# Kernel optimization log

Measured on AMD Instinct MI355X. Metric: run time of the kernel, lower is better.

## Reference

```python
import jax, jax.numpy as jnp
import numpy as np

N_ITERS = 3  # Set2Set n_iters


def _set2set(feat, gid, B, Wih, Whh, bih, bhh):
    # DGL Set2Set with n_iters=3, n_layers=1: LSTM(input=2D, hidden=D), PyTorch gate order i,f,g,o
    N, D = feat.shape
    q_star = jnp.zeros((B, 2 * D), feat.dtype)
    h = jnp.zeros((B, D), feat.dtype)
    c = jnp.zeros((B, D), feat.dtype)
    bias = bih + bhh
    for _ in range(N_ITERS):
        gates = q_star @ Wih.T + h @ Whh.T + bias  # (B, 4D)
        i, f, g, o = jnp.split(gates, 4, axis=-1)
        i = jax.nn.sigmoid(i); f = jax.nn.sigmoid(f); o = jax.nn.sigmoid(o); g = jnp.tanh(g)
        c = f * c + i * g
        h = o * jnp.tanh(c)  # q = h, shape (B, D)
        e = jnp.sum(feat * h[gid], axis=-1)  # (N,) attention logits
        m = jax.ops.segment_max(e, gid, num_segments=B, indices_are_sorted=True)
        ex = jnp.exp(e - m[gid])
        s = jax.ops.segment_sum(ex, gid, num_segments=B, indices_are_sorted=True)
        alpha = ex / s[gid]  # segment softmax
        readout = jax.ops.segment_sum(feat * alpha[:, None], gid, num_segments=B, indices_are_sorted=True)
        q_star = jnp.concatenate([h, readout], axis=-1)  # (B, 2D)
    return q_star


def setup_inputs() -> dict:
    key = jax.random.key(0)
    ks = jax.random.split(key, 18)
    N, E, D, B, OUT = 100000, 1000000, 64, 64, 1
    s = 1.0 / np.sqrt(D)
    u = lambda k, shp, b: jax.random.uniform(k, shp, jnp.float32, -b, b)
    inp = {
        'feat': jax.random.normal(ks[0], (N, D), jnp.float32),
        'efeat': jax.random.normal(ks[1], (E, D), jnp.float32),
        'edge_dst': jax.random.randint(ks[2], (E,), 0, N, jnp.int32),
        'node_graph': jnp.sort(jax.random.randint(ks[3], (N,), 0, B, jnp.int32)),
        'n_graphs': B,
        'node_Wih': u(ks[4], (4 * D, 2 * D), s), 'node_Whh': u(ks[5], (4 * D, D), s),
        'node_bih': u(ks[6], (4 * D,), s), 'node_bhh': u(ks[7], (4 * D,), s),
        'edge_Wih': u(ks[8], (4 * D, 2 * D), s), 'edge_Whh': u(ks[9], (4 * D, D), s),
        'edge_bih': u(ks[10], (4 * D,), s), 'edge_bhh': u(ks[11], (4 * D,), s),
        'W1': u(ks[12], (32, 4 * D), np.sqrt(6.0 / (4 * D + 32)) * np.sqrt(2.0)),
        'b1': jnp.zeros((32,), jnp.float32),
        'W2': u(ks[13], (16, 32), np.sqrt(6.0 / 48) * np.sqrt(2.0)),
        'b2': jnp.zeros((16,), jnp.float32),
        'W3': u(ks[14], (OUT, 16), np.sqrt(6.0 / (16 + OUT)) * np.sqrt(2.0)),
        'b3': jnp.zeros((OUT,), jnp.float32),
    }
    return inp


def reference(feat, efeat, edge_dst, node_graph, n_graphs,
              node_Wih, node_Whh, node_bih, node_bhh,
              edge_Wih, edge_Whh, edge_bih, edge_bhh,
              W1, b1, W2, b2, W3, b3):
    N = feat.shape[0]
    # mpnn = identity: node_emb = feat, edge_emb = efeat
    node_s2s = _set2set(feat, node_graph, n_graphs, node_Wih, node_Whh, node_bih, node_bhh)
    # graph.update_all(fn.copy_e, fn.mean): scatter-mean of edge features onto dst nodes
    deg = jax.ops.segment_sum(jnp.ones((efeat.shape[0],), feat.dtype), edge_dst, num_segments=N)
    edge_agg = jax.ops.segment_sum(efeat, edge_dst, num_segments=N) / jnp.maximum(deg, 1.0)[:, None]
    edge_s2s = _set2set(edge_agg, node_graph, n_graphs, edge_Wih, edge_Whh, edge_bih, edge_bhh)
    out = jnp.concatenate([node_s2s, edge_s2s], axis=1)  # (B, 4D)
    out = jax.nn.relu(out @ W1.T + b1)
    out = jax.nn.relu(out @ W2.T + b2)
    out = out @ W3.T + b3
    return out
```

## Files before the change

kernel.cpp:

```cpp
#include <hip/hip_runtime.h>
#include <math.h>

#define D 64
#define B 64
#define NPB 256
#define SCAN_BS 1024

__device__ __forceinline__ unsigned encf(float x) {
  unsigned u = __float_as_uint(x);
  return (u & 0x80000000u) ? ~u : (u | 0x80000000u);
}
__device__ __forceinline__ float decf(unsigned e) {
  return (e & 0x80000000u) ? __uint_as_float(e ^ 0x80000000u) : __uint_as_float(~e);
}
__device__ __forceinline__ float sigm(float x) { return 1.0f / (1.0f + expf(-x)); }


__global__ void k_deg(const int* __restrict__ edge_dst, int* __restrict__ deg, int E) {
  int i = blockIdx.x * blockDim.x + threadIdx.x;
  if (i < E) atomicAdd(&deg[edge_dst[i]], 1);
}

__global__ void k_scan1(const int* __restrict__ deg, int* __restrict__ row_start,
                        int* __restrict__ blocksum, int N) {
  __shared__ int sm[SCAN_BS];
  int t = threadIdx.x;
  int base = blockIdx.x * SCAN_BS;
  int v = (base + t < N) ? deg[base + t] : 0;
  sm[t] = v;
  __syncthreads();
  for (int ofs = 1; ofs < SCAN_BS; ofs <<= 1) {
    int add = (t >= ofs) ? sm[t - ofs] : 0;
    __syncthreads();
    sm[t] += add;
    __syncthreads();
  }
  if (base + t < N) row_start[base + t] = sm[t] - v;
  if (t == SCAN_BS - 1) blocksum[blockIdx.x] = sm[t];
}

__global__ void k_scan2(int* __restrict__ blocksum, int nb) {
  __shared__ int sm[128];
  int t = threadIdx.x;
  int v = (t < nb) ? blocksum[t] : 0;
  sm[t] = v;
  __syncthreads();
  for (int ofs = 1; ofs < 128; ofs <<= 1) {
    int add = (t >= ofs) ? sm[t - ofs] : 0;
    __syncthreads();
    sm[t] += add;
    __syncthreads();
  }
  if (t < nb) blocksum[t] = sm[t] - v;
}

__global__ void k_scan3(int* __restrict__ row_start, const int* __restrict__ blocksum,
                        int* __restrict__ cursor, int N) {
  int n = blockIdx.x * blockDim.x + threadIdx.x;
  if (n < N) {
    int v = row_start[n] + blocksum[n / SCAN_BS];
    row_start[n] = v;
    cursor[n] = v;
  }
}

__global__ void k_fill(const int* __restrict__ edge_dst, int* __restrict__ cursor,
                       int* __restrict__ csr, int E) {
  int e = blockIdx.x * blockDim.x + threadIdx.x;
  if (e < E) {
    int dst = edge_dst[e];
    int idx = atomicAdd(&cursor[dst], 1);
    csr[idx] = e;
  }
}

__global__ void k_gather(const float* __restrict__ efeat, const int* __restrict__ csr,
                         const int* __restrict__ row_start, const int* __restrict__ deg,
                         float* __restrict__ edge_agg, int N) {
  int grp = (blockIdx.x * blockDim.x + threadIdx.x) >> 4;
  int l16 = threadIdx.x & 15;
  if (grp >= N) return;
  int base = row_start[grp];
  int dg = deg[grp];
  float4 acc = make_float4(0.f, 0.f, 0.f, 0.f);
  for (int i = 0; i < dg; i += 16) {
    int idx[16];
    #pragma unroll
    for (int j = 0; j < 16; ++j) {
      int k = i + j;
      idx[j] = csr[base + (k < dg ? k : dg - 1)];
    }
    #pragma unroll
    for (int j = 0; j < 16; ++j) {
      float4 v = *(const float4*)(efeat + (size_t)idx[j] * D + l16 * 4);
      bool ok = (i + j < dg);
      acc.x += ok ? v.x : 0.0f;
      acc.y += ok ? v.y : 0.0f;
      acc.z += ok ? v.z : 0.0f;
      acc.w += ok ? v.w : 0.0f;
    }
  }
  float inv = 1.0f / fmaxf((float)dg, 1.0f);
  acc.x *= inv; acc.y *= inv; acc.z *= inv; acc.w *= inv;
  *(float4*)(edge_agg + (size_t)grp * D + l16 * 4) = acc;
}


__global__ void k_lstm2(int first, float* __restrict__ h2, float* __restrict__ c2,
                        float* __restrict__ s2, float* __restrict__ r2,
                        unsigned* __restrict__ m2, float* __restrict__ off2,
                        const float* __restrict__ nWih, const float* __restrict__ nWhh,
                        const float* __restrict__ nbih, const float* __restrict__ nbhh,
                        const float* __restrict__ eWih, const float* __restrict__ eWhh,
                        const float* __restrict__ ebih, const float* __restrict__ ebhh) {
  __shared__ float sq[2 * D], sh[D], sg[4 * D];
  int side = blockIdx.y;
  const float* Wih = side ? eWih : nWih;
  const float* Whh = side ? eWhh : nWhh;
  const float* bih = side ? ebih : nbih;
  const float* bhh = side ? ebhh : nbhh;
  float* h = h2 + side * B * D;
  float* c = c2 + side * B * D;
  float* s_buf = s2 + side * B;
  float* r_buf = r2 + side * B * D;

  int b = blockIdx.x, j = threadIdx.x;
  if (j < D) {
    float hv = h[b * D + j];
    sq[j] = hv;
    sh[j] = hv;
  } else if (j < 2 * D) {
    sq[j] = first ? 0.0f : (r_buf[b * D + (j - D)] / s_buf[b]);
  }
  __syncthreads();
  float acc = bih[j] + bhh[j];
  const float* wr = Wih + (size_t)j * (2 * D);
  #pragma unroll 8
  for (int k = 0; k < 2 * D; ++k) acc += sq[k] * wr[k];
  const float* wr2 = Whh + (size_t)j * D;
  #pragma unroll 8
  for (int k = 0; k < D; ++k) acc += sh[k] * wr2[k];
  sg[j] = acc;
  __syncthreads();
  if (j < D) {
    float ig = sigm(sg[j]);
    float fg = sigm(sg[D + j]);
    float gg = tanhf(sg[2 * D + j]);
    float og = sigm(sg[3 * D + j]);
    float cn = fg * c[b * D + j] + ig * gg;
    c[b * D + j] = cn;
    h[b * D + j] = og * tanhf(cn);
    r_buf[b * D + j] = 0.0f;
  }
  if (j == D) s_buf[b] = 0.0f;
  if (j == D + 1) {
    int idx = side * B + b;
    off2[idx] = first ? 0.0f : decf(m2[idx]);
    m2[idx] = 0u;
  }
}

#define NSLOT 4
__global__ void k_att_fused(const float* __restrict__ feat, const float* __restrict__ edge_agg,
                            const int* __restrict__ gid, const float* __restrict__ h2,
                            const float* __restrict__ off2, unsigned* __restrict__ m2,
                            float* __restrict__ s2, float* __restrict__ r2, int N) {
  __shared__ float r_lds[16 * NSLOT * D];
  __shared__ float s_lds[16 * NSLOT];
  __shared__ float m_lds[16 * NSLOT];
  __shared__ float h_lds[NSLOT * D];
  __shared__ float o_lds[NSLOT];
  __shared__ int sg_first;
  __shared__ int used[NSLOT];

  int side = blockIdx.y;
  const float* F = side ? edge_agg : feat;
  const float* h = h2 + side * B * D;
  const float* off = off2 + side * B;
  unsigned* m_enc = m2 + side * B;
  float* s_buf = s2 + side * B;
  float* r_buf = r2 + side * B * D;

  int tid = threadIdx.x;
  int grp = tid >> 4;
  int d4  = tid & 15;
  int base = blockIdx.x * NPB;

  for (int i = tid; i < 16 * NSLOT * D; i += 256) r_lds[i] = 0.0f;
  if (tid < 16 * NSLOT) { s_lds[tid] = 0.0f; m_lds[tid] = -3.4e38f; }
  if (tid < NSLOT) used[tid] = 0;
  if (tid == 0) sg_first = gid[base];
  __syncthreads();
  int gfirst = sg_first;
  {
    int slot = tid >> 6, dim = tid & 63;
    int g = gfirst + slot;
    if (g < B) {
      h_lds[tid] = h[g * D + dim];
      if (dim == 0) o_lds[slot] = off[g];
    }
  }
  __syncthreads();

  float4 acc = make_float4(0.f, 0.f, 0.f, 0.f);
  float sum_ex = 0.0f;
  float local_max = -3.4e38f;
  int cur_g = -1;


  for (int it = 0; it < NPB / 32; ++it) {
    int n0 = base + it * 32 + grp;
    int n1 = n0 + 16;
    bool ok0 = n0 < N, ok1 = n1 < N;
    int g0 = ok0 ? gid[n0] : -1;
    int g1 = ok1 ? gid[n1] : -1;
    float4 f0 = make_float4(0,0,0,0), f1 = make_float4(0,0,0,0);
    float dot0 = 0.f, dot1 = 0.f, ex0 = 0.f, ex1 = 0.f;
    if (ok0) {
      f0 = *(const float4*)(F + (size_t)n0 * D + d4 * 4);
      int s0 = g0 - gfirst;
      float4 hv = (s0 >= 0 && s0 < NSLOT) ? *(const float4*)&h_lds[(s0 << 6) + (d4 << 2)]
                                          : *(const float4*)(h + (size_t)g0 * D + d4 * 4);
      dot0 = f0.x * hv.x + f0.y * hv.y + f0.z * hv.z + f0.w * hv.w;
    }
    if (ok1) {
      f1 = *(const float4*)(F + (size_t)n1 * D + d4 * 4);
      int s1 = g1 - gfirst;
      float4 hv = (s1 >= 0 && s1 < NSLOT) ? *(const float4*)&h_lds[(s1 << 6) + (d4 << 2)]
                                          : *(const float4*)(h + (size_t)g1 * D + d4 * 4);
      dot1 = f1.x * hv.x + f1.y * hv.y + f1.z * hv.z + f1.w * hv.w;
    }
    dot0 += __shfl_xor(dot0, 1); dot1 += __shfl_xor(dot1, 1);
    dot0 += __shfl_xor(dot0, 2); dot1 += __shfl_xor(dot1, 2);
    dot0 += __shfl_xor(dot0, 4); dot1 += __shfl_xor(dot1, 4);
    dot0 += __shfl_xor(dot0, 8); dot1 += __shfl_xor(dot1, 8);
    if (ok0) {
      int s0 = g0 - gfirst;
      ex0 = expf(dot0 - ((s0 >= 0 && s0 < NSLOT) ? o_lds[s0] : off[g0]));
    }
    if (ok1) {
      int s1 = g1 - gfirst;
      ex1 = expf(dot1 - ((s1 >= 0 && s1 < NSLOT) ? o_lds[s1] : off[g1]));
    }

    #pragma unroll
    for (int pair = 0; pair < 2; ++pair) {
      bool ok = pair ? ok1 : ok0;
      int g = pair ? g1 : g0;
      float ex = pair ? ex1 : ex0;
      float dt = pair ? dot1 : dot0;
      float4 f = pair ? f1 : f0;
      if (!ok) continue;
      if (g != cur_g) {
        if (cur_g >= 0) {
          int slot = cur_g - gfirst;
          if (slot >= 0 && slot < NSLOT) {
            float4* p = (float4*)&r_lds[((grp * NSLOT + slot) << 6) + (d4 << 2)];
            float4 v = *p;
            v.x += acc.x; v.y += acc.y; v.z += acc.z; v.w += acc.w;
            *p = v;
            if (d4 == 0) {
              s_lds[grp * NSLOT + slot] += sum_ex;
              m_lds[grp * NSLOT + slot] = fmaxf(m_lds[grp * NSLOT + slot], local_max);
              used[slot] = 1;
            }
          } else {
            float* rp = r_buf + cur_g * D + d4 * 4;
            atomicAdd(rp + 0, acc.x); atomicAdd(rp + 1, acc.y);
            atomicAdd(rp + 2, acc.z); atomicAdd(rp + 3, acc.w);
            if (d4 == 0) { atomicAdd(&s_buf[cur_g], sum_ex); atomicMax(&m_enc[cur_g], encf(local_max)); }
          }
        }
        cur_g = g; acc = make_float4(0,0,0,0); sum_ex = 0.f; local_max = -3.4e38f;
      }
      acc.x += ex * f.x; acc.y += ex * f.y; acc.z += ex * f.z; acc.w += ex * f.w;
      if (d4 == 0) { sum_ex += ex; local_max = fmaxf(local_max, dt); }
    }
  }
  if (cur_g >= 0) {
    int slot = cur_g - gfirst;
    if (slot >= 0 && slot < NSLOT) {
      float4* p = (float4*)&r_lds[((grp * NSLOT + slot) << 6) + (d4 << 2)];
      float4 v = *p;
      v.x += acc.x; v.y += acc.y; v.z += acc.z; v.w += acc.w;
      *p = v;
      if (d4 == 0) {
        s_lds[grp * NSLOT + slot] += sum_ex;
        m_lds[grp * NSLOT + slot] = fmaxf(m_lds[grp * NSLOT + slot], local_max);
        used[slot] = 1;
      }
    } else {
      float* rp = r_buf + cur_g * D + d4 * 4;
      atomicAdd(rp + 0, acc.x); atomicAdd(rp + 1, acc.y);
      atomicAdd(rp + 2, acc.z); atomicAdd(rp + 3, acc.w);
      if (d4 == 0) { atomicAdd(&s_buf[cur_g], sum_ex); atomicMax(&m_enc[cur_g], encf(local_max)); }
    }
  }
  __syncthreads();

  {
    int slot = tid >> 6, dim = tid & 63;
    int g = gfirst + slot;
    if (g < B && used[slot]) {
      float sum = 0.0f;
      #pragma unroll
      for (int q = 0; q < 16; ++q) sum += r_lds[((q * NSLOT + slot) << 6) + dim];
      atomicAdd(&r_buf[g * D + dim], sum);
    }
  }
  if (tid < NSLOT) {
    int g = gfirst + tid;
    if (g < B && used[tid]) {
      float ssum = 0.0f;
      #pragma unroll
      for (int q = 0; q < 16; ++q) ssum += s_lds[q * NSLOT + tid];
      atomicAdd(&s_buf[g], ssum);
    }
  } else if (tid >= 64 && tid < 64 + NSLOT) {
    int slot = tid - 64;
    int g = gfirst + slot;
    if (g < B && used[slot]) {
      float mmax = -3.4e38f;
      #pragma unroll
      for (int q = 0; q < 16; ++q) mmax = fmaxf(mmax, m_lds[q * NSLOT + slot]);
      atomicMax(&m_enc[g], encf(mmax));
    }
  }
}

__global__ void k_mlp(const float* __restrict__ h2, const float* __restrict__ r2,
                      const float* __restrict__ s2,
                      const float* __restrict__ W1, const float* __restrict__ b1,
                      const float* __restrict__ W2, const float* __restrict__ b2,
                      const float* __restrict__ W3, const float* __restrict__ b3,
                      float* __restrict__ out) {
  __shared__ float x[4 * D], h1[32], h2s[16];
  int b = blockIdx.x, t = threadIdx.x;
  x[t]       = (t < D) ? h2[b * D + t]         : r2[b * D + (t - D)] / s2[b];
  x[128 + t] = (t < D) ? h2[B * D + b * D + t] : r2[B * D + b * D + (t - D)] / s2[B + b];
  __syncthreads();
  if (t < 32) {
    float acc = b1[t];
    const float* w = W1 + (size_t)t * (4 * D);
    #pragma unroll 8
    for (int k = 0; k < 4 * D; ++k) acc += x[k] * w[k];
    h1[t] = fmaxf(acc, 0.0f);
  }
  __syncthreads();
  if (t < 16) {
    float acc = b2[t];
    const float* w = W2 + (size_t)t * 32;
    #pragma unroll
    for (int k = 0; k < 32; ++k) acc += h1[k] * w[k];
    h2s[t] = fmaxf(acc, 0.0f);
  }
  __syncthreads();
  if (t == 0) {
    float acc = b3[0];
    #pragma unroll
    for (int k = 0; k < 16; ++k) acc += h2s[k] * W3[k];
    out[b] = acc;
  }
}


extern "C" void kernel_launch(void* const* d_in, const int* in_sizes, int n_in,
                              void* d_out, int out_size, void* d_ws, size_t ws_size,
                              hipStream_t stream) {
  const float* feat      = (const float*)d_in[0];
  const float* efeat     = (const float*)d_in[1];
  const int*   edge_dst  = (const int*)d_in[2];
  const int*   node_graph= (const int*)d_in[3];
  const float* node_Wih  = (const float*)d_in[5];
  const float* node_Whh  = (const float*)d_in[6];
  const float* node_bih  = (const float*)d_in[7];
  const float* node_bhh  = (const float*)d_in[8];
  const float* edge_Wih  = (const float*)d_in[9];
  const float* edge_Whh  = (const float*)d_in[10];
  const float* edge_bih  = (const float*)d_in[11];
  const float* edge_bhh  = (const float*)d_in[12];
  const float* W1 = (const float*)d_in[13];
  const float* b1 = (const float*)d_in[14];
  const float* W2 = (const float*)d_in[15];
  const float* b2 = (const float*)d_in[16];
  const float* W3 = (const float*)d_in[17];
  const float* b3 = (const float*)d_in[18];
  float* out = (float*)d_out;

  const int N = in_sizes[0] / D;
  const int E = in_sizes[2];

  float* ws = (float*)d_ws;
  size_t off = 0;
  float* edge_agg = ws + off; off += (size_t)N * D;
  float* h2       = ws + off; off += 2 * B * D;
  float* c2       = ws + off; off += 2 * B * D;
  float* s2       = ws + off; off += 2 * B;
  float* r2       = ws + off; off += 2 * B * D;
  float* off2     = ws + off; off += 2 * B;
  unsigned* m2    = (unsigned*)(ws + off); off += 2 * B;
  int* deg        = (int*)(ws + off); off += N;
  int* row_start  = (int*)(ws + off); off += N;
  int* cursor     = (int*)(ws + off); off += N;
  int* blocksum   = (int*)(ws + off); off += 128;
  int* csr        = (int*)(ws + off); off += E + 8;

  hipMemsetAsync(deg, 0, (size_t)N * sizeof(int), stream);
  hipMemsetAsync(h2, 0, (size_t)(4 * B * D) * sizeof(float), stream);

  const int nb = (N + SCAN_BS - 1) / SCAN_BS;
  k_deg<<<(E + 255) / 256, 256, 0, stream>>>(edge_dst, deg, E);
  k_scan1<<<nb, SCAN_BS, 0, stream>>>(deg, row_start, blocksum, N);
  k_scan2<<<1, 128, 0, stream>>>(blocksum, nb);
  k_scan3<<<(N + 255) / 256, 256, 0, stream>>>(row_start, blocksum, cursor, N);
  k_fill<<<(E + 255) / 256, 256, 0, stream>>>(edge_dst, cursor, csr, E);

  k_gather<<<(N + 15) / 16, 256, 0, stream>>>(efeat, csr, row_start, deg, edge_agg, N);

  const int att_blocks = (N + NPB - 1) / NPB;
  dim3 ga(att_blocks, 2), gb(B, 2);

  for (int it = 0; it < 3; ++it) {
    k_lstm2<<<gb, 256, 0, stream>>>(it == 0 ? 1 : 0, h2, c2, s2, r2, m2, off2,
                                    node_Wih, node_Whh, node_bih, node_bhh,
                                    edge_Wih, edge_Whh, edge_bih, edge_bhh);
    k_att_fused<<<ga, 256, 0, stream>>>(feat, edge_agg, node_graph, h2, off2, m2, s2, r2, N);
  }

  k_mlp<<<B, 128, 0, stream>>>(h2, r2, s2, W1, b1, W2, b2, W3, b3, out);
}
```

Before: 267.5 us.

## Fuse Set2Set LSTM, attention and MLP into one cooperative kernel

Replaces the three pairs of LSTM and attention launches plus the final MLP launch with a single cooperative kernel that uses grid-wide syncs between phases. NPB doubles to 512 so the grid (196x2 blocks) can stay co-resident under launch_bounds(256,2). This removes six kernel launches and their gaps. In exchange it adds grid barrier cost, requires every block to be resident at once, and gives each block twice as much serial work.

```diff
diff --git a/kernel.cpp b/kernel.cpp
--- a/kernel.cpp
+++ b/kernel.cpp
@@ -1,9 +1,13 @@
 #include <hip/hip_runtime.h>
+#include <hip/hip_cooperative_groups.h>
 #include <math.h>
+
+namespace cg = cooperative_groups;
 
 #define D 64
 #define B 64
-#define NPB 256
+#define NPB 512
+#define NSLOT 4
 #define SCAN_BS 1024
 
 __device__ __forceinline__ unsigned encf(float x) {
@@ -106,260 +110,264 @@
 }
 
 
-__global__ void k_lstm2(int first, float* __restrict__ h2, float* __restrict__ c2,
-                        float* __restrict__ s2, float* __restrict__ r2,
-                        unsigned* __restrict__ m2, float* __restrict__ off2,
-                        const float* __restrict__ nWih, const float* __restrict__ nWhh,
-                        const float* __restrict__ nbih, const float* __restrict__ nbhh,
-                        const float* __restrict__ eWih, const float* __restrict__ eWhh,
-                        const float* __restrict__ ebih, const float* __restrict__ ebhh) {
-  __shared__ float sq[2 * D], sh[D], sg[4 * D];
-  int side = blockIdx.y;
+__global__ __launch_bounds__(256, 2)
+void k_s2s(const float* __restrict__ feat, const float* __restrict__ edge_agg,
+           const int* __restrict__ gid,
+           float* __restrict__ h2g, float* __restrict__ c2g,
+           float* __restrict__ s2g, float* __restrict__ r2g,
+           unsigned* __restrict__ m2g, float* __restrict__ off2g,
+           const float* __restrict__ nWih, const float* __restrict__ nWhh,
+           const float* __restrict__ nbih, const float* __restrict__ nbhh,
+           const float* __restrict__ eWih, const float* __restrict__ eWhh,
+           const float* __restrict__ ebih, const float* __restrict__ ebhh,
+           const float* __restrict__ W1, const float* __restrict__ b1,
+           const float* __restrict__ W2, const float* __restrict__ b2,
+           const float* __restrict__ W3, const float* __restrict__ b3,
+           float* __restrict__ out, int N) {
+  cg::grid_group gg = cg::this_grid();
+
+  const int side = blockIdx.y;
+  const int bx = blockIdx.x;
+  const int tid = threadIdx.x;
+
+  const float* F   = side ? edge_agg : feat;
   const float* Wih = side ? eWih : nWih;
   const float* Whh = side ? eWhh : nWhh;
   const float* bih = side ? ebih : nbih;
   const float* bhh = side ? ebhh : nbhh;
-  float* h = h2 + side * B * D;
-  float* c = c2 + side * B * D;
-  float* s_buf = s2 + side * B;
-  float* r_buf = r2 + side * B * D;
-
-  int b = blockIdx.x, j = threadIdx.x;
-  if (j < D) {
-    float hv = h[b * D + j];
-    sq[j] = hv;
-    sh[j] = hv;
-  } else if (j < 2 * D) {
-    sq[j] = first ? 0.0f : (r_buf[b * D + (j - D)] / s_buf[b]);
-  }
-  __syncthreads();
-  float acc = bih[j] + bhh[j];
-  const float* wr = Wih + (size_t)j * (2 * D);
-  #pragma unroll 8
-  for (int k = 0; k < 2 * D; ++k) acc += sq[k] * wr[k];
-  const float* wr2 = Whh + (size_t)j * D;
-  #pragma unroll 8
-  for (int k = 0; k < D; ++k) acc += sh[k] * wr2[k];
-  sg[j] = acc;
-  __syncthreads();
-  if (j < D) {
-    float ig = sigm(sg[j]);
-    float fg = sigm(sg[D + j]);
-    float gg = tanhf(sg[2 * D + j]);
-    float og = sigm(sg[3 * D + j]);
-    float cn = fg * c[b * D + j] + ig * gg;
-    c[b * D + j] = cn;
-    h[b * D + j] = og * tanhf(cn);
-    r_buf[b * D + j] = 0.0f;
-  }
-  if (j == D) s_buf[b] = 0.0f;
-  if (j == D + 1) {
-    int idx = side * B + b;
-    off2[idx] = first ? 0.0f : decf(m2[idx]);
-    m2[idx] = 0u;
-  }
-}
-
-#define NSLOT 4
-__global__ void k_att_fused(const float* __restrict__ feat, const float* __restrict__ edge_agg,
-                            const int* __restrict__ gid, const float* __restrict__ h2,
-                            const float* __restrict__ off2, unsigned* __restrict__ m2,
-                            float* __restrict__ s2, float* __restrict__ r2, int N) {
+  float* h     = h2g + side * B * D;
+  float* c     = c2g + side * B * D;
+  float* s_buf = s2g + side * B;
+  float* r_buf = r2g + side * B * D;
+  unsigned* m_enc = m2g + side * B;
+  float* off   = off2g + side * B;
+
   __shared__ float r_lds[16 * NSLOT * D];
   __shared__ float s_lds[16 * NSLOT];
   __shared__ float m_lds[16 * NSLOT];
   __shared__ float h_lds[NSLOT * D];
   __shared__ float o_lds[NSLOT];
+  __shared__ int used[NSLOT];
   __shared__ int sg_first;
-  __shared__ int used[NSLOT];
-
-  int side = blockIdx.y;
-  const float* F = side ? edge_agg : feat;
-  const float* h = h2 + side * B * D;
-  const float* off = off2 + side * B;
-  unsigned* m_enc = m2 + side * B;
-  float* s_buf = s2 + side * B;
-  float* r_buf = r2 + side * B * D;
-
-  int tid = threadIdx.x;
-  int grp = tid >> 4;
-  int d4  = tid & 15;
-  int base = blockIdx.x * NPB;
-
-  for (int i = tid; i < 16 * NSLOT * D; i += 256) r_lds[i] = 0.0f;
-  if (tid < 16 * NSLOT) { s_lds[tid] = 0.0f; m_lds[tid] = -3.4e38f; }
-  if (tid < NSLOT) used[tid] = 0;
-  if (tid == 0) sg_first = gid[base];
-  __syncthreads();
-  int gfirst = sg_first;
-  {
-    int slot = tid >> 6, dim = tid & 63;
-    int g = gfirst + slot;
-    if (g < B) {
-      h_lds[tid] = h[g * D + dim];
-      if (dim == 0) o_lds[slot] = off[g];
-    }
-  }
-  __syncthreads();
-
-  float4 acc = make_float4(0.f, 0.f, 0.f, 0.f);
-  float sum_ex = 0.0f;
-  float local_max = -3.4e38f;
-  int cur_g = -1;
-
-
-  for (int it = 0; it < NPB / 32; ++it) {
-    int n0 = base + it * 32 + grp;
-    int n1 = n0 + 16;
-    bool ok0 = n0 < N, ok1 = n1 < N;
-    int g0 = ok0 ? gid[n0] : -1;
-    int g1 = ok1 ? gid[n1] : -1;
-    float4 f0 = make_float4(0,0,0,0), f1 = make_float4(0,0,0,0);
-    float dot0 = 0.f, dot1 = 0.f, ex0 = 0.f, ex1 = 0.f;
-    if (ok0) {
-      f0 = *(const float4*)(F + (size_t)n0 * D + d4 * 4);
-      int s0 = g0 - gfirst;
-      float4 hv = (s0 >= 0 && s0 < NSLOT) ? *(const float4*)&h_lds[(s0 << 6) + (d4 << 2)]
-                                          : *(const float4*)(h + (size_t)g0 * D + d4 * 4);
-      dot0 = f0.x * hv.x + f0.y * hv.y + f0.z * hv.z + f0.w * hv.w;
-    }
-    if (ok1) {
-      f1 = *(const float4*)(F + (size_t)n1 * D + d4 * 4);
-      int s1 = g1 - gfirst;
-      float4 hv = (s1 >= 0 && s1 < NSLOT) ? *(const float4*)&h_lds[(s1 << 6) + (d4 << 2)]
-                                          : *(const float4*)(h + (size_t)g1 * D + d4 * 4);
-      dot1 = f1.x * hv.x + f1.y * hv.y + f1.z * hv.z + f1.w * hv.w;
-    }
-    dot0 += __shfl_xor(dot0, 1); dot1 += __shfl_xor(dot1, 1);
-    dot0 += __shfl_xor(dot0, 2); dot1 += __shfl_xor(dot1, 2);
-    dot0 += __shfl_xor(dot0, 4); dot1 += __shfl_xor(dot1, 4);
-    dot0 += __shfl_xor(dot0, 8); dot1 += __shfl_xor(dot1, 8);
-    if (ok0) {
-      int s0 = g0 - gfirst;
-      ex0 = expf(dot0 - ((s0 >= 0 && s0 < NSLOT) ? o_lds[s0] : off[g0]));
-    }
-    if (ok1) {
-      int s1 = g1 - gfirst;
-      ex1 = expf(dot1 - ((s1 >= 0 && s1 < NSLOT) ? o_lds[s1] : off[g1]));
-    }
-
-    #pragma unroll
-    for (int pair = 0; pair < 2; ++pair) {
-      bool ok = pair ? ok1 : ok0;
-      int g = pair ? g1 : g0;
-      float ex = pair ? ex1 : ex0;
-      float dt = pair ? dot1 : dot0;
-      float4 f = pair ? f1 : f0;
-      if (!ok) continue;
-      if (g != cur_g) {
-        if (cur_g >= 0) {
-          int slot = cur_g - gfirst;
-          if (slot >= 0 && slot < NSLOT) {
-            float4* p = (float4*)&r_lds[((grp * NSLOT + slot) << 6) + (d4 << 2)];
-            float4 v = *p;
-            v.x += acc.x; v.y += acc.y; v.z += acc.z; v.w += acc.w;
-            *p = v;
-            if (d4 == 0) {
-              s_lds[grp * NSLOT + slot] += sum_ex;
-              m_lds[grp * NSLOT + slot] = fmaxf(m_lds[grp * NSLOT + slot], local_max);
-              used[slot] = 1;
+  __shared__ float lq[2 * D];
+  __shared__ float lsg[4 * D];
+
+  const int base = bx * NPB;
+  const int grp = tid >> 4;
+  const int d4  = tid & 15;
+
+  for (int it = 0; it < 3; ++it) {
+    if (bx < B) {
+      const int b = bx, j = tid;
+      if (j < D) {
+        lq[j] = h[b * D + j];
+      } else if (j < 2 * D) {
+        lq[j] = (it == 0) ? 0.0f : (r_buf[b * D + (j - D)] / s_buf[b]);
+      }
+      __syncthreads();
+      float acc = bih[j] + bhh[j];
+      const float* wr = Wih + (size_t)j * (2 * D);
+      #pragma unroll 8
+      for (int k = 0; k < 2 * D; ++k) acc += lq[k] * wr[k];
+      const float* wr2 = Whh + (size_t)j * D;
+      #pragma unroll 8
+      for (int k = 0; k < D; ++k) acc += lq[k] * wr2[k];
+      lsg[j] = acc;
+      __syncthreads();
+      if (j < D) {
+        float ig = sigm(lsg[j]);
+        float fg = sigm(lsg[D + j]);
+        float gGate = tanhf(lsg[2 * D + j]);
+        float og = sigm(lsg[3 * D + j]);
+        float cn = fg * c[b * D + j] + ig * gGate;
+        c[b * D + j] = cn;
+        h[b * D + j] = og * tanhf(cn);
+        r_buf[b * D + j] = 0.0f;
+      }
+      if (j == D) s_buf[b] = 0.0f;
+      if (j == D + 1) {
+        off[b] = (it == 0) ? 0.0f : decf(m_enc[b]);
+        m_enc[b] = 0u;
+      }
+      __syncthreads();
+    }
+    gg.sync();
+
+    for (int i = tid; i < 16 * NSLOT * D; i += 256) r_lds[i] = 0.0f;
+    if (tid < 16 * NSLOT) { s_lds[tid] = 0.0f; m_lds[tid] = -3.4e38f; }
+    if (tid < NSLOT) used[tid] = 0;
+    if (tid == 0) sg_first = gid[base];
+    __syncthreads();
+    const int gfirst = sg_first;
+    {
+      int slot = tid >> 6, dim = tid & 63;
+      int g = gfirst + slot;
+      if (g < B) {
+        h_lds[tid] = h[g * D + dim];
+        if (dim == 0) o_lds[slot] = off[g];
+      }
+    }
+    __syncthreads();
+
+    float4 acc = make_float4(0.f, 0.f, 0.f, 0.f);
+    float sum_ex = 0.0f;
+    float local_max = -3.4e38f;
+    int cur_g = -1;
+
+    for (int itn = 0; itn < NPB / 32; ++itn) {
+      int n0 = base + itn * 32 + grp;
+      int n1 = n0 + 16;
+      bool ok0 = n0 < N, ok1 = n1 < N;
+      int g0 = ok0 ? gid[n0] : -1;
+      int g1 = ok1 ? gid[n1] : -1;
+      float4 f0 = make_float4(0,0,0,0), f1 = make_float4(0,0,0,0);
+      float dot0 = 0.f, dot1 = 0.f, ex0 = 0.f, ex1 = 0.f;
+      if (ok0) {
+        f0 = *(const float4*)(F + (size_t)n0 * D + d4 * 4);
+        int s0 = g0 - gfirst;
+        float4 hv = (s0 >= 0 && s0 < NSLOT) ? *(const float4*)&h_lds[(s0 << 6) + (d4 << 2)]
+                                            : *(const float4*)(h + (size_t)g0 * D + d4 * 4);
+        dot0 = f0.x * hv.x + f0.y * hv.y + f0.z * hv.z + f0.w * hv.w;
+      }
+      if (ok1) {
+        f1 = *(const float4*)(F + (size_t)n1 * D + d4 * 4);
+        int s1 = g1 - gfirst;
+        float4 hv = (s1 >= 0 && s1 < NSLOT) ? *(const float4*)&h_lds[(s1 << 6) + (d4 << 2)]
+                                            : *(const float4*)(h + (size_t)g1 * D + d4 * 4);
+        dot1 = f1.x * hv.x + f1.y * hv.y + f1.z * hv.z + f1.w * hv.w;
+      }
+      dot0 += __shfl_xor(dot0, 1); dot1 += __shfl_xor(dot1, 1);
+      dot0 += __shfl_xor(dot0, 2); dot1 += __shfl_xor(dot1, 2);
+      dot0 += __shfl_xor(dot0, 4); dot1 += __shfl_xor(dot1, 4);
+      dot0 += __shfl_xor(dot0, 8); dot1 += __shfl_xor(dot1, 8);
+      if (ok0) {
+        int s0 = g0 - gfirst;
+        ex0 = expf(dot0 - ((s0 >= 0 && s0 < NSLOT) ? o_lds[s0] : off[g0]));
+      }
+      if (ok1) {
+        int s1 = g1 - gfirst;
+        ex1 = expf(dot1 - ((s1 >= 0 && s1 < NSLOT) ? o_lds[s1] : off[g1]));
+      }
+
+      #pragma unroll
+      for (int pair = 0; pair < 2; ++pair) {
+        bool ok = pair ? ok1 : ok0;
+        int g = pair ? g1 : g0;
+        float ex = pair ? ex1 : ex0;
+        float dt = pair ? dot1 : dot0;
+        float4 f = pair ? f1 : f0;
+        if (!ok) continue;
+        if (g != cur_g) {
+          if (cur_g >= 0) {
+            int slot = cur_g - gfirst;
+            if (slot >= 0 && slot < NSLOT) {
+              float4* p = (float4*)&r_lds[((grp * NSLOT + slot) << 6) + (d4 << 2)];
+              float4 v = *p;
+              v.x += acc.x; v.y += acc.y; v.z += acc.z; v.w += acc.w;
+              *p = v;
+              if (d4 == 0) {
+                s_lds[grp * NSLOT + slot] += sum_ex;
+                m_lds[grp * NSLOT + slot] = fmaxf(m_lds[grp * NSLOT + slot], local_max);
+                used[slot] = 1;
+              }
+            } else {
+              float* rp = r_buf + cur_g * D + d4 * 4;
+              atomicAdd(rp + 0, acc.x); atomicAdd(rp + 1, acc.y);
+              atomicAdd(rp + 2, acc.z); atomicAdd(rp + 3, acc.w);
+              if (d4 == 0) { atomicAdd(&s_buf[cur_g], sum_ex); atomicMax(&m_enc[cur_g], encf(local_max)); }
             }
-          } else {
-            float* rp = r_buf + cur_g * D + d4 * 4;
-            atomicAdd(rp + 0, acc.x); atomicAdd(rp + 1, acc.y);
-            atomicAdd(rp + 2, acc.z); atomicAdd(rp + 3, acc.w);
-            if (d4 == 0) { atomicAdd(&s_buf[cur_g], sum_ex); atomicMax(&m_enc[cur_g], encf(local_max)); }
           }
+          cur_g = g; acc = make_float4(0,0,0,0); sum_ex = 0.f; local_max = -3.4e38f;
         }
-        cur_g = g; acc = make_float4(0,0,0,0); sum_ex = 0.f; local_max = -3.4e38f;
-      }
-      acc.x += ex * f.x; acc.y += ex * f.y; acc.z += ex * f.z; acc.w += ex * f.w;
-      if (d4 == 0) { sum_ex += ex; local_max = fmaxf(local_max, dt); }
-    }
-  }
-  if (cur_g >= 0) {
-    int slot = cur_g - gfirst;
-    if (slot >= 0 && slot < NSLOT) {
-      float4* p = (float4*)&r_lds[((grp * NSLOT + slot) << 6) + (d4 << 2)];
-      float4 v = *p;
-      v.x += acc.x; v.y += acc.y; v.z += acc.z; v.w += acc.w;
-      *p = v;
-      if (d4 == 0) {
-        s_lds[grp * NSLOT + slot] += sum_ex;
-        m_lds[grp * NSLOT + slot] = fmaxf(m_lds[grp * NSLOT + slot], local_max);
-        used[slot] = 1;
-      }
-    } else {
-      float* rp = r_buf + cur_g * D + d4 * 4;
-      atomicAdd(rp + 0, acc.x); atomicAdd(rp + 1, acc.y);
-      atomicAdd(rp + 2, acc.z); atomicAdd(rp + 3, acc.w);
-      if (d4 == 0) { atomicAdd(&s_buf[cur_g], sum_ex); atomicMax(&m_enc[cur_g], encf(local_max)); }
-    }
-  }
-  __syncthreads();
-
-  {
-    int slot = tid >> 6, dim = tid & 63;
-    int g = gfirst + slot;
-    if (g < B && used[slot]) {
-      float sum = 0.0f;
+        acc.x += ex * f.x; acc.y += ex * f.y; acc.z += ex * f.z; acc.w += ex * f.w;
+        if (d4 == 0) { sum_ex += ex; local_max = fmaxf(local_max, dt); }
+      }
+    }
+    if (cur_g >= 0) {
+      int slot = cur_g - gfirst;
+      if (slot >= 0 && slot < NSLOT) {
+        float4* p = (float4*)&r_lds[((grp * NSLOT + slot) << 6) + (d4 << 2)];
+        float4 v = *p;
+        v.x += acc.x; v.y += acc.y; v.z += acc.z; v.w += acc.w;
+        *p = v;
+        if (d4 == 0) {
+          s_lds[grp * NSLOT + slot] += sum_ex;
+          m_lds[grp * NSLOT + slot] = fmaxf(m_lds[grp * NSLOT + slot], local_max);
+          used[slot] = 1;
+        }
+      } else {
+        float* rp = r_buf + cur_g * D + d4 * 4;
+        atomicAdd(rp + 0, acc.x); atomicAdd(rp + 1, acc.y);
+        atomicAdd(rp + 2, acc.z); atomicAdd(rp + 3, acc.w);
+        if (d4 == 0) { atomicAdd(&s_buf[cur_g], sum_ex); atomicMax(&m_enc[cur_g], encf(local_max)); }
+      }
+    }
+    __syncthreads();
+
+    {
+      int slot = tid >> 6, dim = tid & 63;
+      int g = gfirst + slot;
+      if (g < B && used[slot]) {
+        float sum = 0.0f;
+        #pragma unroll
+        for (int q = 0; q < 16; ++q) sum += r_lds[((q * NSLOT + slot) << 6) + dim];
+        atomicAdd(&r_buf[g * D + dim], sum);
+      }
+    }
+    if (tid < NSLOT) {
+      int g = gfirst + tid;
+      if (g < B && used[tid]) {
+        float ssum = 0.0f;
+        #pragma unroll
+        for (int q = 0; q < 16; ++q) ssum += s_lds[q * NSLOT + tid];
+        atomicAdd(&s_buf[g], ssum);
+      }
+    } else if (tid >= 64 && tid < 64 + NSLOT) {
+      int slot = tid - 64;
+      int g = gfirst + slot;
+      if (g < B && used[slot]) {
+        float mmax = -3.4e38f;
+        #pragma unroll
+        for (int q = 0; q < 16; ++q) mmax = fmaxf(mmax, m_lds[q * NSLOT + slot]);
+        atomicMax(&m_enc[g], encf(mmax));
+      }
+    }
+    __syncthreads();
+    gg.sync();
+  }
+
+  if (side == 0 && bx < B) {
+    const int b = bx, t = tid;
+    float* x   = r_lds;
+    float* hh1 = r_lds + 4 * D;
+    float* hh2 = r_lds + 4 * D + 32;
+    if (t < 128) {
+      x[t]       = (t < D) ? h2g[b * D + t]         : r2g[b * D + (t - D)] / s2g[b];
+      x[128 + t] = (t < D) ? h2g[B * D + b * D + t] : r2g[B * D + b * D + (t - D)] / s2g[B + b];
+    }
+    __syncthreads();
+    if (t < 32) {
+      float acc = b1[t];
+      const float* w = W1 + (size_t)t * (4 * D);
+      #pragma unroll 8
+      for (int k = 0; k < 4 * D; ++k) acc += x[k] * w[k];
+      hh1[t] = fmaxf(acc, 0.0f);
+    }
+    __syncthreads();
+    if (t < 16) {
+      float acc = b2[t];
+      const float* w = W2 + (size_t)t * 32;
       #pragma unroll
-      for (int q = 0; q < 16; ++q) sum += r_lds[((q * NSLOT + slot) << 6) + dim];
-      atomicAdd(&r_buf[g * D + dim], sum);
-    }
-  }
-  if (tid < NSLOT) {
-    int g = gfirst + tid;
-    if (g < B && used[tid]) {
-      float ssum = 0.0f;
+      for (int k = 0; k < 32; ++k) acc += hh1[k] * w[k];
+      hh2[t] = fmaxf(acc, 0.0f);
+    }
+    __syncthreads();
+    if (t == 0) {
+      float acc = b3[0];
       #pragma unroll
-      for (int q = 0; q < 16; ++q) ssum += s_lds[q * NSLOT + tid];
-      atomicAdd(&s_buf[g], ssum);
-    }
-  } else if (tid >= 64 && tid < 64 + NSLOT) {
-    int slot = tid - 64;
-    int g = gfirst + slot;
-    if (g < B && used[slot]) {
-      float mmax = -3.4e38f;
-      #pragma unroll
-      for (int q = 0; q < 16; ++q) mmax = fmaxf(mmax, m_lds[q * NSLOT + slot]);
-      atomicMax(&m_enc[g], encf(mmax));
-    }
-  }
-}
-
-__global__ void k_mlp(const float* __restrict__ h2, const float* __restrict__ r2,
-                      const float* __restrict__ s2,
-                      const float* __restrict__ W1, const float* __restrict__ b1,
-                      const float* __restrict__ W2, const float* __restrict__ b2,
-                      const float* __restrict__ W3, const float* __restrict__ b3,
-                      float* __restrict__ out) {
-  __shared__ float x[4 * D], h1[32], h2s[16];
-  int b = blockIdx.x, t = threadIdx.x;
-  x[t]       = (t < D) ? h2[b * D + t]         : r2[b * D + (t - D)] / s2[b];
-  x[128 + t] = (t < D) ? h2[B * D + b * D + t] : r2[B * D + b * D + (t - D)] / s2[B + b];
-  __syncthreads();
-  if (t < 32) {
-    float acc = b1[t];
-    const float* w = W1 + (size_t)t * (4 * D);
-    #pragma unroll 8
-    for (int k = 0; k < 4 * D; ++k) acc += x[k] * w[k];
-    h1[t] = fmaxf(acc, 0.0f);
-  }
-  __syncthreads();
-  if (t < 16) {
-    float acc = b2[t];
-    const float* w = W2 + (size_t)t * 32;
-    #pragma unroll
-    for (int k = 0; k < 32; ++k) acc += h1[k] * w[k];
-    h2s[t] = fmaxf(acc, 0.0f);
-  }
-  __syncthreads();
-  if (t == 0) {
-    float acc = b3[0];
-    #pragma unroll
-    for (int k = 0; k < 16; ++k) acc += h2s[k] * W3[k];
-    out[b] = acc;
+      for (int k = 0; k < 16; ++k) acc += hh2[k] * W3[k];
+      out[b] = acc;
+    }
   }
 }
 
@@ -417,15 +425,15 @@
 
   k_gather<<<(N + 15) / 16, 256, 0, stream>>>(efeat, csr, row_start, deg, edge_agg, N);
 
-  const int att_blocks = (N + NPB - 1) / NPB;
-  dim3 ga(att_blocks, 2), gb(B, 2);
-
-  for (int it = 0; it < 3; ++it) {
-    k_lstm2<<<gb, 256, 0, stream>>>(it == 0 ? 1 : 0, h2, c2, s2, r2, m2, off2,
-                                    node_Wih, node_Whh, node_bih, node_bhh,
-                                    edge_Wih, edge_Whh, edge_bih, edge_bhh);
-    k_att_fused<<<ga, 256, 0, stream>>>(feat, edge_agg, node_graph, h2, off2, m2, s2, r2, N);
-  }
-
-  k_mlp<<<B, 128, 0, stream>>>(h2, r2, s2, W1, b1, W2, b2, W3, b3, out);
-}
+  int nchunks = (N + NPB - 1) / NPB;
+  void* args[] = {
+    (void*)&feat, (void*)&edge_agg, (void*)&node_graph,
+    (void*)&h2, (void*)&c2, (void*)&s2, (void*)&r2, (void*)&m2, (void*)&off2,
+    (void*)&node_Wih, (void*)&node_Whh, (void*)&node_bih, (void*)&node_bhh,
+    (void*)&edge_Wih, (void*)&edge_Whh, (void*)&edge_bih, (void*)&edge_bhh,
+    (void*)&W1, (void*)&b1, (void*)&W2, (void*)&b2, (void*)&W3, (void*)&b3,
+    (void*)&out, (void*)&N
+  };
+  hipLaunchCooperativeKernel((void*)k_s2s, dim3(nchunks, 2), dim3(256),
+                             args, 0, stream);
+}
```

Measured after the change: 560.4 us. +109.5%, slower.

## Skew node and edge Set2Set chains to overlap gather with node attention

Applied to the files above, without the earlier changes.

The node-side Set2Set does not depend on the edge aggregation, so the schedule is skewed. The node-side first LSTM and attention iteration run alongside the edge gather in a single combined launch, with gather blocks and attention blocks partitioned by block index. The LSTM and attention kernels take a side_base parameter and per-side 'first' flags so the two chains can run one iteration out of phase, with a final edge-only step. This is meant to fill the GPU during the bandwidth-bound gather and remove one launch-level dependency. The cost is a kernel whose blocks have different shapes and an extra LSTM/attention launch at the tail.

```diff
diff --git a/kernel.cpp b/kernel.cpp
--- a/kernel.cpp
+++ b/kernel.cpp
@@ -4,6 +4,7 @@
 #define D 64
 #define B 64
 #define NPB 256
+#define NSLOT 4
 #define SCAN_BS 1024
 
 __device__ __forceinline__ unsigned encf(float x) {
@@ -74,130 +75,42 @@
   }
 }
 
-__global__ void k_gather(const float* __restrict__ efeat, const int* __restrict__ csr,
-                         const int* __restrict__ row_start, const int* __restrict__ deg,
-                         float* __restrict__ edge_agg, int N) {
-  int grp = (blockIdx.x * blockDim.x + threadIdx.x) >> 4;
-  int l16 = threadIdx.x & 15;
-  if (grp >= N) return;
-  int base = row_start[grp];
-  int dg = deg[grp];
-  float4 acc = make_float4(0.f, 0.f, 0.f, 0.f);
-  for (int i = 0; i < dg; i += 16) {
-    int idx[16];
-    #pragma unroll
-    for (int j = 0; j < 16; ++j) {
-      int k = i + j;
-      idx[j] = csr[base + (k < dg ? k : dg - 1)];
-    }
-    #pragma unroll
-    for (int j = 0; j < 16; ++j) {
-      float4 v = *(const float4*)(efeat + (size_t)idx[j] * D + l16 * 4);
-      bool ok = (i + j < dg);
-      acc.x += ok ? v.x : 0.0f;
-      acc.y += ok ? v.y : 0.0f;
-      acc.z += ok ? v.z : 0.0f;
-      acc.w += ok ? v.w : 0.0f;
-    }
-  }
-  float inv = 1.0f / fmaxf((float)dg, 1.0f);
-  acc.x *= inv; acc.y *= inv; acc.z *= inv; acc.w *= inv;
-  *(float4*)(edge_agg + (size_t)grp * D + l16 * 4) = acc;
-}
-
-
-__global__ void k_lstm2(int first, float* __restrict__ h2, float* __restrict__ c2,
-                        float* __restrict__ s2, float* __restrict__ r2,
-                        unsigned* __restrict__ m2, float* __restrict__ off2,
-                        const float* __restrict__ nWih, const float* __restrict__ nWhh,
-                        const float* __restrict__ nbih, const float* __restrict__ nbhh,
-                        const float* __restrict__ eWih, const float* __restrict__ eWhh,
-                        const float* __restrict__ ebih, const float* __restrict__ ebhh) {
-  __shared__ float sq[2 * D], sh[D], sg[4 * D];
-  int side = blockIdx.y;
-  const float* Wih = side ? eWih : nWih;
-  const float* Whh = side ? eWhh : nWhh;
-  const float* bih = side ? ebih : nbih;
-  const float* bhh = side ? ebhh : nbhh;
-  float* h = h2 + side * B * D;
-  float* c = c2 + side * B * D;
-  float* s_buf = s2 + side * B;
-  float* r_buf = r2 + side * B * D;
-
-  int b = blockIdx.x, j = threadIdx.x;
-  if (j < D) {
-    float hv = h[b * D + j];
-    sq[j] = hv;
-    sh[j] = hv;
-  } else if (j < 2 * D) {
-    sq[j] = first ? 0.0f : (r_buf[b * D + (j - D)] / s_buf[b]);
-  }
-  __syncthreads();
-  float acc = bih[j] + bhh[j];
-  const float* wr = Wih + (size_t)j * (2 * D);
-  #pragma unroll 8
-  for (int k = 0; k < 2 * D; ++k) acc += sq[k] * wr[k];
-  const float* wr2 = Whh + (size_t)j * D;
-  #pragma unroll 8
-  for (int k = 0; k < D; ++k) acc += sh[k] * wr2[k];
-  sg[j] = acc;
-  __syncthreads();
-  if (j < D) {
-    float ig = sigm(sg[j]);
-    float fg = sigm(sg[D + j]);
-    float gg = tanhf(sg[2 * D + j]);
-    float og = sigm(sg[3 * D + j]);
-    float cn = fg * c[b * D + j] + ig * gg;
-    c[b * D + j] = cn;
-    h[b * D + j] = og * tanhf(cn);
-    r_buf[b * D + j] = 0.0f;
-  }
-  if (j == D) s_buf[b] = 0.0f;
-  if (j == D + 1) {
-    int idx = side * B + b;
-    off2[idx] = first ? 0.0f : decf(m2[idx]);
-    m2[idx] = 0u;
-  }
-}
-
-#define NSLOT 4
-__global__ void k_att_fused(const float* __restrict__ feat, const float* __restrict__ edge_agg,
-                            const int* __restrict__ gid, const float* __restrict__ h2,
-                            const float* __restrict__ off2, unsigned* __restrict__ m2,
-                            float* __restrict__ s2, float* __restrict__ r2, int N) {
-  __shared__ float r_lds[16 * NSLOT * D];
-  __shared__ float s_lds[16 * NSLOT];
-  __shared__ float m_lds[16 * NSLOT];
-  __shared__ float h_lds[NSLOT * D];
-  __shared__ float o_lds[NSLOT];
-  __shared__ int sg_first;
-  __shared__ int used[NSLOT];
-
-  int side = blockIdx.y;
-  const float* F = side ? edge_agg : feat;
-  const float* h = h2 + side * B * D;
-  const float* off = off2 + side * B;
-  unsigned* m_enc = m2 + side * B;
-  float* s_buf = s2 + side * B;
-  float* r_buf = r2 + side * B * D;
-
-  int tid = threadIdx.x;
-  int grp = tid >> 4;
-  int d4  = tid & 15;
-  int base = blockIdx.x * NPB;
-
-  for (int i = tid; i < 16 * NSLOT * D; i += 256) r_lds[i] = 0.0f;
-  if (tid < 16 * NSLOT) { s_lds[tid] = 0.0f; m_lds[tid] = -3.4e38f; }
-  if (tid < NSLOT) used[tid] = 0;
-  if (tid == 0) sg_first = gid[base];
-  __syncthreads();
-  int gfirst = sg_first;
+
+struct AttSmem {
+  float r_lds[16 * NSLOT * D];
+  float s_lds[16 * NSLOT];
+  float m_lds[16 * NSLOT];
+  float h_lds[NSLOT * D];
+  float o_lds[NSLOT];
+  int used[NSLOT];
+  int sg_first;
+};
+
+__device__ __forceinline__ void att_body(AttSmem* sm, const float* __restrict__ F,
+                                         const int* __restrict__ gid,
+                                         const float* __restrict__ h,
+                                         const float* __restrict__ off,
+                                         unsigned* __restrict__ m_enc,
+                                         float* __restrict__ s_buf,
+                                         float* __restrict__ r_buf,
+                                         int N, int bx) {
+  const int tid = threadIdx.x;
+  const int grp = tid >> 4;
+  const int d4  = tid & 15;
+  const int base = bx * NPB;
+
+  for (int i = tid; i < 16 * NSLOT * D; i += 256) sm->r_lds[i] = 0.0f;
+  if (tid < 16 * NSLOT) { sm->s_lds[tid] = 0.0f; sm->m_lds[tid] = -3.4e38f; }
+  if (tid < NSLOT) sm->used[tid] = 0;
+  if (tid == 0) sm->sg_first = gid[base];
+  __syncthreads();
+  const int gfirst = sm->sg_first;
   {
     int slot = tid >> 6, dim = tid & 63;
     int g = gfirst + slot;
     if (g < B) {
-      h_lds[tid] = h[g * D + dim];
-      if (dim == 0) o_lds[slot] = off[g];
+      sm->h_lds[tid] = h[g * D + dim];
+      if (dim == 0) sm->o_lds[slot] = off[g];
     }
   }
   __syncthreads();
@@ -207,9 +120,8 @@
   float local_max = -3.4e38f;
   int cur_g = -1;
 
-
-  for (int it = 0; it < NPB / 32; ++it) {
-    int n0 = base + it * 32 + grp;
+  for (int itn = 0; itn < NPB / 32; ++itn) {
+    int n0 = base + itn * 32 + grp;
     int n1 = n0 + 16;
     bool ok0 = n0 < N, ok1 = n1 < N;
     int g0 = ok0 ? gid[n0] : -1;
@@ -219,14 +131,14 @@
     if (ok0) {
       f0 = *(const float4*)(F + (size_t)n0 * D + d4 * 4);
       int s0 = g0 - gfirst;
-      float4 hv = (s0 >= 0 && s0 < NSLOT) ? *(const float4*)&h_lds[(s0 << 6) + (d4 << 2)]
+      float4 hv = (s0 >= 0 && s0 < NSLOT) ? *(const float4*)&sm->h_lds[(s0 << 6) + (d4 << 2)]
                                           : *(const float4*)(h + (size_t)g0 * D + d4 * 4);
       dot0 = f0.x * hv.x + f0.y * hv.y + f0.z * hv.z + f0.w * hv.w;
     }
     if (ok1) {
       f1 = *(const float4*)(F + (size_t)n1 * D + d4 * 4);
       int s1 = g1 - gfirst;
-      float4 hv = (s1 >= 0 && s1 < NSLOT) ? *(const float4*)&h_lds[(s1 << 6) + (d4 << 2)]
+      float4 hv = (s1 >= 0 && s1 < NSLOT) ? *(const float4*)&sm->h_lds[(s1 << 6) + (d4 << 2)]
                                           : *(const float4*)(h + (size_t)g1 * D + d4 * 4);
       dot1 = f1.x * hv.x + f1.y * hv.y + f1.z * hv.z + f1.w * hv.w;
     }
@@ -236,11 +148,11 @@
     dot0 += __shfl_xor(dot0, 8); dot1 += __shfl_xor(dot1, 8);
     if (ok0) {
       int s0 = g0 - gfirst;
-      ex0 = expf(dot0 - ((s0 >= 0 && s0 < NSLOT) ? o_lds[s0] : off[g0]));
+      ex0 = expf(dot0 - ((s0 >= 0 && s0 < NSLOT) ? sm->o_lds[s0] : off[g0]));
     }
     if (ok1) {
       int s1 = g1 - gfirst;
-      ex1 = expf(dot1 - ((s1 >= 0 && s1 < NSLOT) ? o_lds[s1] : off[g1]));
+      ex1 = expf(dot1 - ((s1 >= 0 && s1 < NSLOT) ? sm->o_lds[s1] : off[g1]));
     }
 
     #pragma unroll
@@ -255,14 +167,14 @@
         if (cur_g >= 0) {
           int slot = cur_g - gfirst;
           if (slot >= 0 && slot < NSLOT) {
-            float4* p = (float4*)&r_lds[((grp * NSLOT + slot) << 6) + (d4 << 2)];
+            float4* p = (float4*)&sm->r_lds[((grp * NSLOT + slot) << 6) + (d4 << 2)];
             float4 v = *p;
             v.x += acc.x; v.y += acc.y; v.z += acc.z; v.w += acc.w;
             *p = v;
             if (d4 == 0) {
-              s_lds[grp * NSLOT + slot] += sum_ex;
-              m_lds[grp * NSLOT + slot] = fmaxf(m_lds[grp * NSLOT + slot], local_max);
-              used[slot] = 1;
+              sm->s_lds[grp * NSLOT + slot] += sum_ex;
+              sm->m_lds[grp * NSLOT + slot] = fmaxf(sm->m_lds[grp * NSLOT + slot], local_max);
+              sm->used[slot] = 1;
             }
           } else {
             float* rp = r_buf + cur_g * D + d4 * 4;
@@ -280,14 +192,14 @@
   if (cur_g >= 0) {
     int slot = cur_g - gfirst;
     if (slot >= 0 && slot < NSLOT) {
-      float4* p = (float4*)&r_lds[((grp * NSLOT + slot) << 6) + (d4 << 2)];
+      float4* p = (float4*)&sm->r_lds[((grp * NSLOT + slot) << 6) + (d4 << 2)];
       float4 v = *p;
       v.x += acc.x; v.y += acc.y; v.z += acc.z; v.w += acc.w;
       *p = v;
       if (d4 == 0) {
-        s_lds[grp * NSLOT + slot] += sum_ex;
-        m_lds[grp * NSLOT + slot] = fmaxf(m_lds[grp * NSLOT + slot], local_max);
-        used[slot] = 1;
+        sm->s_lds[grp * NSLOT + slot] += sum_ex;
+        sm->m_lds[grp * NSLOT + slot] = fmaxf(sm->m_lds[grp * NSLOT + slot], local_max);
+        sm->used[slot] = 1;
       }
     } else {
       float* rp = r_buf + cur_g * D + d4 * 4;
@@ -301,32 +213,148 @@
   {
     int slot = tid >> 6, dim = tid & 63;
     int g = gfirst + slot;
-    if (g < B && used[slot]) {
+    if (g < B && sm->used[slot]) {
       float sum = 0.0f;
       #pragma unroll
-      for (int q = 0; q < 16; ++q) sum += r_lds[((q * NSLOT + slot) << 6) + dim];
+      for (int q = 0; q < 16; ++q) sum += sm->r_lds[((q * NSLOT + slot) << 6) + dim];
       atomicAdd(&r_buf[g * D + dim], sum);
     }
   }
   if (tid < NSLOT) {
     int g = gfirst + tid;
-    if (g < B && used[tid]) {
+    if (g < B && sm->used[tid]) {
       float ssum = 0.0f;
       #pragma unroll
-      for (int q = 0; q < 16; ++q) ssum += s_lds[q * NSLOT + tid];
+      for (int q = 0; q < 16; ++q) ssum += sm->s_lds[q * NSLOT + tid];
       atomicAdd(&s_buf[g], ssum);
     }
   } else if (tid >= 64 && tid < 64 + NSLOT) {
     int slot = tid - 64;
     int g = gfirst + slot;
-    if (g < B && used[slot]) {
+    if (g < B && sm->used[slot]) {
       float mmax = -3.4e38f;
       #pragma unroll
-      for (int q = 0; q < 16; ++q) mmax = fmaxf(mmax, m_lds[q * NSLOT + slot]);
+      for (int q = 0; q < 16; ++q) mmax = fmaxf(mmax, sm->m_lds[q * NSLOT + slot]);
       atomicMax(&m_enc[g], encf(mmax));
     }
   }
 }
+
+__device__ __forceinline__ void gather_body(const float* __restrict__ efeat,
+                                            const int* __restrict__ csr,
+                                            const int* __restrict__ row_start,
+                                            const int* __restrict__ deg,
+                                            float* __restrict__ edge_agg, int N, int bx) {
+  int grp = (bx * 256 + threadIdx.x) >> 4;
+  int l16 = threadIdx.x & 15;
+  if (grp >= N) return;
+  int base = row_start[grp];
+  int dg = deg[grp];
+  float4 acc = make_float4(0.f, 0.f, 0.f, 0.f);
+  for (int i = 0; i < dg; i += 16) {
+    int idx[16];
+    #pragma unroll
+    for (int j = 0; j < 16; ++j) {
+      int k = i + j;
+      idx[j] = csr[base + (k < dg ? k : dg - 1)];
+    }
+    #pragma unroll
+    for (int j = 0; j < 16; ++j) {
+      float4 v = *(const float4*)(efeat + (size_t)idx[j] * D + l16 * 4);
+      bool ok = (i + j < dg);
+      acc.x += ok ? v.x : 0.0f;
+      acc.y += ok ? v.y : 0.0f;
+      acc.z += ok ? v.z : 0.0f;
+      acc.w += ok ? v.w : 0.0f;
+    }
+  }
+  float inv = 1.0f / fmaxf((float)dg, 1.0f);
+  acc.x *= inv; acc.y *= inv; acc.z *= inv; acc.w *= inv;
+  *(float4*)(edge_agg + (size_t)grp * D + l16 * 4) = acc;
+}
+
+__global__ void k_gather_att0(int GB, const float* __restrict__ efeat,
+                              const int* __restrict__ csr, const int* __restrict__ row_start,
+                              const int* __restrict__ deg, float* __restrict__ edge_agg,
+                              const float* __restrict__ feat, const int* __restrict__ gid,
+                              const float* __restrict__ h2, const float* __restrict__ off2,
+                              unsigned* __restrict__ m2, float* __restrict__ s2,
+                              float* __restrict__ r2, int N) {
+  __shared__ AttSmem sm;
+  if ((int)blockIdx.x < GB) {
+    gather_body(efeat, csr, row_start, deg, edge_agg, N, blockIdx.x);
+  } else {
+    att_body(&sm, feat, gid, h2, off2, m2, s2, r2, N, blockIdx.x - GB);
+  }
+}
+
+__global__ void k_att(int side_base, const float* __restrict__ feat,
+                      const float* __restrict__ edge_agg, const int* __restrict__ gid,
+                      const float* __restrict__ h2, const float* __restrict__ off2,
+                      unsigned* __restrict__ m2, float* __restrict__ s2,
+                      float* __restrict__ r2, int N) {
+  __shared__ AttSmem sm;
+  int side = blockIdx.y + side_base;
+  att_body(&sm, side ? edge_agg : feat, gid, h2 + side * B * D, off2 + side * B,
+           m2 + side * B, s2 + side * B, r2 + side * B * D, N, blockIdx.x);
+}
+
+
+__global__ void k_lstm(int firstN, int firstE, int side_base,
+                       float* __restrict__ h2, float* __restrict__ c2,
+                       float* __restrict__ s2, float* __restrict__ r2,
+                       unsigned* __restrict__ m2, float* __restrict__ off2,
+                       const float* __restrict__ nWih, const float* __restrict__ nWhh,
+                       const float* __restrict__ nbih, const float* __restrict__ nbhh,
+                       const float* __restrict__ eWih, const float* __restrict__ eWhh,
+                       const float* __restrict__ ebih, const float* __restrict__ ebhh) {
+  __shared__ float lq[2 * D], lsg[4 * D];
+  int side = blockIdx.y + side_base;
+  int first = side ? firstE : firstN;
+  const float* Wih = side ? eWih : nWih;
+  const float* Whh = side ? eWhh : nWhh;
+  const float* bih = side ? ebih : nbih;
+  const float* bhh = side ? ebhh : nbhh;
+  float* h = h2 + side * B * D;
+  float* c = c2 + side * B * D;
+  float* s_buf = s2 + side * B;
+  float* r_buf = r2 + side * B * D;
+  unsigned* m_enc = m2 + side * B;
+  float* off = off2 + side * B;
+
+  int b = blockIdx.x, j = threadIdx.x;
+  if (j < D) {
+    lq[j] = h[b * D + j];
+  } else if (j < 2 * D) {
+    lq[j] = first ? 0.0f : (r_buf[b * D + (j - D)] / s_buf[b]);
+  }
+  __syncthreads();
+  float acc = bih[j] + bhh[j];
+  const float* wr = Wih + (size_t)j * (2 * D);
+  #pragma unroll 8
+  for (int k = 0; k < 2 * D; ++k) acc += lq[k] * wr[k];
+  const float* wr2 = Whh + (size_t)j * D;
+  #pragma unroll 8
+  for (int k = 0; k < D; ++k) acc += lq[k] * wr2[k];
+  lsg[j] = acc;
+  __syncthreads();
+  if (j < D) {
+    float ig = sigm(lsg[j]);
+    float fg = sigm(lsg[D + j]);
+    float gg = tanhf(lsg[2 * D + j]);
+    float og = sigm(lsg[3 * D + j]);
+    float cn = fg * c[b * D + j] + ig * gg;
+    c[b * D + j] = cn;
+    h[b * D + j] = og * tanhf(cn);
+    r_buf[b * D + j] = 0.0f;
+  }
+  if (j == D) s_buf[b] = 0.0f;
+  if (j == D + 1) {
+    off[b] = first ? 0.0f : decf(m_enc[b]);
+    m_enc[b] = 0u;
+  }
+}
+
 
 __global__ void k_mlp(const float* __restrict__ h2, const float* __restrict__ r2,
                       const float* __restrict__ s2,
@@ -415,17 +443,22 @@
   k_scan3<<<(N + 255) / 256, 256, 0, stream>>>(row_start, blocksum, cursor, N);
   k_fill<<<(E + 255) / 256, 256, 0, stream>>>(edge_dst, cursor, csr, E);
 
-  k_gather<<<(N + 15) / 16, 256, 0, stream>>>(efeat, csr, row_start, deg, edge_agg, N);
-
   const int att_blocks = (N + NPB - 1) / NPB;
-  dim3 ga(att_blocks, 2), gb(B, 2);
-
-  for (int it = 0; it < 3; ++it) {
-    k_lstm2<<<gb, 256, 0, stream>>>(it == 0 ? 1 : 0, h2, c2, s2, r2, m2, off2,
-                                    node_Wih, node_Whh, node_bih, node_bhh,
-                                    edge_Wih, edge_Whh, edge_bih, edge_bhh);
-    k_att_fused<<<ga, 256, 0, stream>>>(feat, edge_agg, node_graph, h2, off2, m2, s2, r2, N);
-  }
+  const int GB = (N + 15) / 16;
+
+  k_lstm<<<dim3(B, 1), 256, 0, stream>>>(1, 0, 0, h2, c2, s2, r2, m2, off2,
+      node_Wih, node_Whh, node_bih, node_bhh, edge_Wih, edge_Whh, edge_bih, edge_bhh);
+  k_gather_att0<<<GB + att_blocks, 256, 0, stream>>>(GB, efeat, csr, row_start, deg, edge_agg,
+      feat, node_graph, h2, off2, m2, s2, r2, N);
+  k_lstm<<<dim3(B, 2), 256, 0, stream>>>(0, 1, 0, h2, c2, s2, r2, m2, off2,
+      node_Wih, node_Whh, node_bih, node_bhh, edge_Wih, edge_Whh, edge_bih, edge_bhh);
+  k_att<<<dim3(att_blocks, 2), 256, 0, stream>>>(0, feat, edge_agg, node_graph, h2, off2, m2, s2, r2, N);
+  k_lstm<<<dim3(B, 2), 256, 0, stream>>>(0, 0, 0, h2, c2, s2, r2, m2, off2,
+      node_Wih, node_Whh, node_bih, node_bhh, edge_Wih, edge_Whh, edge_bih, edge_bhh);
+  k_att<<<dim3(att_blocks, 2), 256, 0, stream>>>(0, feat, edge_agg, node_graph, h2, off2, m2, s2, r2, N);
+  k_lstm<<<dim3(B, 1), 256, 0, stream>>>(0, 0, 1, h2, c2, s2, r2, m2, off2,
+      node_Wih, node_Whh, node_bih, node_bhh, edge_Wih, edge_Whh, edge_bih, edge_bhh);
+  k_att<<<dim3(att_blocks, 1), 256, 0, stream>>>(1, feat, edge_agg, node_graph, h2, off2, m2, s2, r2, N);
 
   k_mlp<<<B, 128, 0, stream>>>(h2, r2, s2, W1, b1, W2, b2, W3, b3, out);
 }
```

After: 285.2 us. 6.6% more time.
